# Performance work log

Hardware: AMD Instinct MI355X
Metric: run time of the kernel (lower is better)

## Reference

```python
import jax, jax.numpy as jnp
import numpy as np

B, L, D, H = 2, 2048, 1024, 16
DH = D // H  # 64

def setup_inputs() -> dict:
    key = jax.random.key(0)
    ks = jax.random.split(key, 5)
    s = 1.0 / np.sqrt(D)
    return {
        "x": jax.random.normal(ks[0], (B, L, D), jnp.float32),
        "Wk": jax.random.normal(ks[1], (D, D), jnp.float32) * s,
        "Wq": jax.random.normal(ks[2], (D, D), jnp.float32) * s,
        "Wv": jax.random.normal(ks[3], (D, D), jnp.float32) * s,
        "Wo": jax.random.normal(ks[4], (D, D), jnp.float32) * s,
    }

def reference(x, Wk, Wq, Wv, Wo):
    # Linear(D,D,bias=False): y = x @ W.T ; W stored [out,in] as in torch
    k = (x @ Wk.T).reshape(B, L, H, DH).transpose(0, 2, 1, 3)  # [B,H,L,dh]
    q = (x @ Wq.T).reshape(B, L, H, DH).transpose(0, 2, 1, 3)
    v = (x @ Wv.T).reshape(B, L, H, DH).transpose(0, 2, 1, 3)
    att = jnp.einsum("bhqd,bhkd->bhqk", q, k) / jnp.sqrt(jnp.float32(DH))
    causal = jnp.tril(jnp.ones((L, L), dtype=bool))
    att = jnp.where(causal, att, -jnp.inf)
    p = jax.nn.softmax(att, axis=-1)  # dropout omitted (eval mode)
    out = jnp.einsum("bhqk,bhkd->bhqd", p, v)  # [B,H,L,dh]
    out = out.transpose(0, 2, 1, 3).reshape(B, L, D)
    return out @ Wo.T
```

## Files before the change

### kernel.cpp

```cpp
#include <hip/hip_runtime.h>

typedef __bf16 bf16_t;
typedef __bf16 bf16x8 __attribute__((ext_vector_type(8)));
typedef __bf16 bf16x4 __attribute__((ext_vector_type(4)));
typedef float f32x4 __attribute__((ext_vector_type(4)));

#define MFMA_BF16(a, b, c) __builtin_amdgcn_mfma_f32_16x16x32_bf16((a), (b), (c), 0, 0, 0)
#define LOG2E 1.44269504088896f

__device__ __forceinline__ void gload16(const bf16_t* g, bf16_t* l) {
  __builtin_amdgcn_global_load_lds(
      (__attribute__((address_space(1))) void*)(g),
      (__attribute__((address_space(3))) void*)(l), 16, 0, 0);
}

__global__ void cast_all(const float* __restrict__ x, const float* __restrict__ wk,
                         const float* __restrict__ wq, const float* __restrict__ wv,
                         const float* __restrict__ wo, bf16_t* __restrict__ xbf,
                         bf16_t* __restrict__ wbf) {
  const size_t NX = 4194304, NW = 1048576;
  size_t i = (size_t)blockIdx.x * blockDim.x + threadIdx.x;
  const size_t total4 = (NX + 4 * NW) / 4;
  const size_t stride = (size_t)gridDim.x * blockDim.x;
  for (; i < total4; i += stride) {
    size_t f = i * 4;
    const float* src;
    bf16_t* dst;
    if (f < NX) {
      src = x + f;
      dst = xbf + f;
    } else {
      size_t g = f - NX;
      size_t wsel = g >> 20;
      size_t off = g & (NW - 1);
      dst = wbf + g;
      src = (wsel == 0) ? wq + off : (wsel == 1) ? wk + off : (wsel == 2) ? wv + off : wo + off;
    }
    float4 v = *(const float4*)src;
    bf16x4 o;
    o[0] = (bf16_t)v.x; o[1] = (bf16_t)v.y; o[2] = (bf16_t)v.z; o[3] = (bf16_t)v.w;
    *(bf16x4*)dst = o;
  }
}

template <int BM, int BN, typename TOUT>
__global__ __launch_bounds__(256) void gemm_nt(const bf16_t* __restrict__ A,
                                               const bf16_t* __restrict__ W,
                                               TOUT* __restrict__ C, int K, int ldc,
                                               int blocksPerSect, bf16_t* __restrict__ vtb) {
  constexpr int MF = BM / 32;
  constexpr int NF = BN / 32;
  __shared__ bf16_t As[BM * 64];
  __shared__ bf16_t Bs[BN * 64];
  const int t = threadIdx.x;
  const int l = t & 63, w = t >> 6;
  const int wm = w >> 1;
  const int wn = w & 1;
  const int lr = l & 15, lg = l >> 4;
  const int bm = blockIdx.x;
  const int by = blockIdx.y;
  const int sect = by / blocksPerSect;
  const int bn = by - sect * blocksPerSect;
  const bf16_t* Wp = W + ((size_t)sect << 20);
  const int n0 = sect * 1024 + bn * BN;

  const int srow0 = t >> 3;
  const int csw = (t & 7) ^ (srow0 & 7);
  const bf16_t* ag = A + (size_t)(bm * BM + srow0) * K + csw * 8;
  const bf16_t* bg = Wp + (size_t)(bn * BN + srow0) * K + csw * 8;

  f32x4 acc[MF][NF];
#pragma unroll
  for (int i = 0; i < MF; ++i)
#pragma unroll
    for (int j = 0; j < NF; ++j) acc[i][j] = (f32x4){0.f, 0.f, 0.f, 0.f};

  for (int k0 = 0; k0 < K; k0 += 64) {
    __syncthreads();
#pragma unroll
    for (int p = 0; p < BM / 32; ++p) gload16(ag + (size_t)(32 * p) * K, As + t * 8 + p * 2048);
#pragma unroll
    for (int p = 0; p < BN / 32; ++p) gload16(bg + (size_t)(32 * p) * K, Bs + t * 8 + p * 2048);
    ag += 64;
    bg += 64;
    __syncthreads();
#pragma unroll
    for (int kk = 0; kk < 2; ++kk) {
      bf16x8 af[MF], bfr[NF];
#pragma unroll
      for (int mf = 0; mf < MF; ++mf) {
        int row = wm * (MF * 16) + mf * 16 + lr;
        af[mf] = *(const bf16x8*)(As + row * 64 + (((kk * 4 + lg) ^ (row & 7)) * 8));
      }
#pragma unroll
      for (int nf = 0; nf < NF; ++nf) {
        int row = wn * (NF * 16) + nf * 16 + lr;
        bfr[nf] = *(const bf16x8*)(Bs + row * 64 + (((kk * 4 + lg) ^ (row & 7)) * 8));
      }
#pragma unroll
      for (int mf = 0; mf < MF; ++mf)
#pragma unroll
        for (int nf = 0; nf < NF; ++nf)
          acc[mf][nf] = MFMA_BF16(af[mf], bfr[nf], acc[mf][nf]);
    }
  }

  if (vtb != nullptr && sect == 2) {
#pragma unroll
    for (int mf = 0; mf < MF; ++mf)
#pragma unroll
      for (int nf = 0; nf < NF; ++nf) {
        int row0 = bm * BM + wm * (MF * 16) + mf * 16 + lg * 4;
        int colg = bn * BN + wn * (NF * 16) + nf * 16 + lr;
        int bb = row0 >> 11, ll = row0 & 2047;
        size_t vaddr = ((size_t)((bb * 16 + (colg >> 6)) * 64 + (colg & 63))) * 2048 + ll;
        bf16x4 pk;
#pragma unroll
        for (int j = 0; j < 4; ++j) pk[j] = (bf16_t)acc[mf][nf][j];
        *(bf16x4*)(vtb + vaddr) = pk;
      }
    return;
  }
#pragma unroll
  for (int mf = 0; mf < MF; ++mf)
#pragma unroll
    for (int nf = 0; nf < NF; ++nf)
#pragma unroll
      for (int j = 0; j < 4; ++j) {
        int row = bm * BM + wm * (MF * 16) + mf * 16 + lg * 4 + j;
        int col = n0 + wn * (NF * 16) + nf * 16 + lr;
        C[(size_t)row * ldc + col] = (TOUT)acc[mf][nf][j];
      }
}

__global__ __launch_bounds__(256, 4) void attn_fwd(const bf16_t* __restrict__ qk,
                                                   const bf16_t* __restrict__ vt,
                                                   bf16_t* __restrict__ out) {
  __shared__ bf16_t Ks[2][4096];
  __shared__ bf16_t Vts[2][4096];
  __shared__ bf16_t Pt[4][1024];
  const int t = threadIdx.x, l = t & 63, w = t >> 6;
  const int lr = l & 15, lg = l >> 4;
  const int n = blockIdx.x;
  const int bh = n & 31;
  const int b = bh >> 4, h = bh & 15;
  const int m = n >> 5;
  const int j8 = m & 7, kk = m >> 3;
  const int qt = (kk == 0) ? j8 : (kk == 1) ? 15 - j8 : (kk == 2) ? 16 + j8 : 31 - j8;
  const int qloc = w * 16 + lr;
  const int qrow = qt * 64 + qloc;

  const float SCINIT = -12.f * LOG2E;

  const int srow = t >> 3, sc8 = t & 7;
  const int cs = sc8 ^ (srow & 7);
  const bf16_t* kbase = qk + ((size_t)(b * 2048 + srow)) * 2048 + 1024 + h * 64 + cs * 8;
  const bf16_t* vbase = vt + ((size_t)(bh * 64 + srow)) * 2048 + cs * 8;
  char* Ks0 = (char*)&Ks[0][0];
  char* Vt0 = (char*)&Vts[0][0];
  const int stg = t * 16;

#define STAGE(ktile, sboff)                                                   \
  do {                                                                        \
    const bf16_t* ks_ = kbase + (size_t)(ktile) * (64 * 2048);                \
    const bf16_t* vs_ = vbase + (size_t)(ktile) * 64;                         \
    gload16(ks_, (bf16_t*)(Ks0 + (sboff) + stg));                             \
    gload16(ks_ + (size_t)32 * 2048, (bf16_t*)(Ks0 + (sboff) + 4096 + stg));  \
    gload16(vs_, (bf16_t*)(Vt0 + (sboff) + stg));                             \
    gload16(vs_ + (size_t)32 * 2048, (bf16_t*)(Vt0 + (sboff) + 4096 + stg));  \
  } while (0)

  const float qsc = 0.125f * LOG2E;
  const bf16_t* Qg = qk + (size_t)(b * 2048 + qrow) * 2048 + h * 64 + lg * 8;
  bf16x8 qf0 = *(const bf16x8*)(Qg);
  bf16x8 qf1 = *(const bf16x8*)(Qg + 32);
#pragma unroll
  for (int jj = 0; jj < 8; ++jj) {
    qf0[jj] = (bf16_t)((float)qf0[jj] * qsc);
    qf1[jj] = (bf16_t)((float)qf1[jj] * qsc);
  }

  f32x4 acc[4];
#pragma unroll
  for (int df = 0; df < 4; ++df) acc[df] = (f32x4){0.f, 0.f, 0.f, 0.f};
  float l_r = 0.f;

  const int r7 = lr & 7;
  const int o0 = lr * 128 + ((lg ^ r7) * 16);
  const int o1 = lr * 128 + (((lg ^ 4) ^ r7) * 16);

  char* PwB = (char*)&Pt[w][0];
  const int psw = r7 << 4;
  int pwo[4];
#pragma unroll
  for (int nf = 0; nf < 4; ++nf) pwo[nf] = lr * 128 + ((nf * 32 + lg * 8) ^ psw);
  const int pr0 = lr * 128 + ((lg * 16) ^ psw);
  const int pr1 = lr * 128 + ((64 + lg * 16) ^ psw);

  STAGE(0, 0);
  __syncthreads();

  int boff = 0;
  for (int kt = 0; kt <= qt; ++kt) {
    if (kt < qt) STAGE(kt + 1, boff ^ 8192);

    f32x4 sc[4];
#pragma unroll
    for (int nf = 0; nf < 4; ++nf)
      sc[nf] = (f32x4){SCINIT, SCINIT, SCINIT, SCINIT};
    __builtin_amdgcn_s_setprio(1);
#pragma unroll
    for (int nf = 0; nf < 4; ++nf) {
      bf16x8 kf0 = *(const bf16x8*)(Ks0 + boff + nf * 2048 + o0);
      bf16x8 kf1 = *(const bf16x8*)(Ks0 + boff + nf * 2048 + o1);
      sc[nf] = MFMA_BF16(kf0, qf0, sc[nf]);
      sc[nf] = MFMA_BF16(kf1, qf1, sc[nf]);
    }
    __builtin_amdgcn_s_setprio(0);

    float p[16], ps = 0.f;
    if (kt == qt) {
#pragma unroll
      for (int nf = 0; nf < 4; ++nf)
#pragma unroll
        for (int jj = 0; jj < 4; ++jj) {
          float sv = sc[nf][jj];
          if (nf * 16 + lg * 4 + jj > qloc) sv = -1e30f;
          float pv = __builtin_amdgcn_exp2f(sv);
          p[nf * 4 + jj] = pv;
          ps += pv;
        }
    } else {
#pragma unroll
      for (int nf = 0; nf < 4; ++nf)
#pragma unroll
        for (int jj = 0; jj < 4; ++jj) {
          float pv = __builtin_amdgcn_exp2f(sc[nf][jj]);
          p[nf * 4 + jj] = pv;
          ps += pv;
        }
    }
    l_r += ps;

#pragma unroll
    for (int nf = 0; nf < 4; ++nf) {
      bf16x4 pk;
#pragma unroll
      for (int jj = 0; jj < 4; ++jj) pk[jj] = (bf16_t)p[nf * 4 + jj];
      *(bf16x4*)(PwB + pwo[nf]) = pk;
    }

    bf16x8 pb0 = *(const bf16x8*)(PwB + pr0);
    bf16x8 pb1 = *(const bf16x8*)(PwB + pr1);
    __builtin_amdgcn_s_setprio(1);
#pragma unroll
    for (int df = 0; df < 4; ++df) {
      bf16x8 vf0 = *(const bf16x8*)(Vt0 + boff + df * 2048 + o0);
      bf16x8 vf1 = *(const bf16x8*)(Vt0 + boff + df * 2048 + o1);
      acc[df] = MFMA_BF16(vf0, pb0, acc[df]);
      acc[df] = MFMA_BF16(vf1, pb1, acc[df]);
    }
    __builtin_amdgcn_s_setprio(0);
    __syncthreads();
    boff ^= 8192;
  }
#undef STAGE

  l_r += __shfl_xor(l_r, 16);
  l_r += __shfl_xor(l_r, 32);
  float inv = 1.f / l_r;
#pragma unroll
  for (int df = 0; df < 4; ++df) {
    bf16x4 o;
#pragma unroll
    for (int jj = 0; jj < 4; ++jj) o[jj] = (bf16_t)(acc[df][jj] * inv);
    *(bf16x4*)(out + (size_t)(b * 2048 + qrow) * 1024 + h * 64 + df * 16 + lg * 4) = o;
  }
}

extern "C" void kernel_launch(void* const* d_in, const int* in_sizes, int n_in,
                              void* d_out, int out_size, void* d_ws, size_t ws_size,
                              hipStream_t stream) {
  const float* x = (const float*)d_in[0];
  const float* wk = (const float*)d_in[1];
  const float* wq = (const float*)d_in[2];
  const float* wv = (const float*)d_in[3];
  const float* wo = (const float*)d_in[4];

  bf16_t* xbf = (bf16_t*)d_ws;
  bf16_t* wbf = xbf + 4194304;
  bf16_t* qkbf = wbf + 4194304;
  bf16_t* vtbuf = qkbf + 8388608;
  bf16_t* attnbf = xbf;
  float* out = (float*)d_out;

  cast_all<<<dim3(2048), dim3(256), 0, stream>>>(x, wk, wq, wv, wo, xbf, wbf);
  gemm_nt<128, 64, bf16_t><<<dim3(32, 48), dim3(256), 0, stream>>>(xbf, wbf, qkbf, 1024, 2048, 16,
                                                                   vtbuf);
  attn_fwd<<<dim3(1024), dim3(256), 0, stream>>>(qkbf, vtbuf, attnbf);
  gemm_nt<64, 64, float><<<dim3(64, 16), dim3(256), 0, stream>>>(attnbf, wbf + 3 * 1048576, out,
                                                                 1024, 1024, 16, (bf16_t*)nullptr);
}
```

Measured before the change: 102.4 us.

## Double-buffer GEMM LDS tiles with K-step 32 and prefetch next stage

Changes the projection GEMM main loop from a single-buffered 64-wide K tile to two 32-wide K tile buffers. The next stage's global-to-LDS loads are issued before computing on the current buffer, leaving one barrier per iteration. This aims to overlap memory latency with MFMA work. In exchange it halves the MFMA work per iteration, doubles the iteration count and changes the LDS swizzle.

```diff
diff --git a/kernel.cpp b/kernel.cpp
--- a/kernel.cpp
+++ b/kernel.cpp
@@ -50,8 +50,10 @@
                                                int blocksPerSect, bf16_t* __restrict__ vtb) {
   constexpr int MF = BM / 32;
   constexpr int NF = BN / 32;
-  __shared__ bf16_t As[BM * 64];
-  __shared__ bf16_t Bs[BN * 64];
+  constexpr int ABYTES = BM * 64;
+  constexpr int BBYTES = BN * 64;
+  __shared__ bf16_t As[2][BM * 32];
+  __shared__ bf16_t Bs[2][BN * 32];
   const int t = threadIdx.x;
   const int l = t & 63, w = t >> 6;
   const int wm = w >> 1;
@@ -64,10 +66,25 @@
   const bf16_t* Wp = W + ((size_t)sect << 20);
   const int n0 = sect * 1024 + bn * BN;
 
-  const int srow0 = t >> 3;
-  const int csw = (t & 7) ^ (srow0 & 7);
+  const int srow0 = t >> 2;
+  const int csw = (t & 3) ^ ((t >> 3) & 3);
   const bf16_t* ag = A + (size_t)(bm * BM + srow0) * K + csw * 8;
   const bf16_t* bg = Wp + (size_t)(bn * BN + srow0) * K + csw * 8;
+  char* As0 = (char*)&As[0][0];
+  char* Bs0 = (char*)&Bs[0][0];
+  const int stg = t * 16;
+
+#define GSTAGE(k0, sb)                                                                   \
+  do {                                                                                   \
+    _Pragma("unroll") for (int p = 0; p < BM / 64; ++p)                                  \
+        gload16(ag + (size_t)(64 * p) * K + (k0), (bf16_t*)(As0 + (sb)*ABYTES + p * 4096 + stg)); \
+    _Pragma("unroll") for (int p = 0; p < BN / 64; ++p)                                  \
+        gload16(bg + (size_t)(64 * p) * K + (k0), (bf16_t*)(Bs0 + (sb)*BBYTES + p * 4096 + stg)); \
+  } while (0)
+
+  const int off = lr * 64 + ((lg ^ ((lr >> 1) & 3)) * 16);
+  const int abase = wm * (MF * 1024) + off;
+  const int bbase = wn * (NF * 1024) + off;
 
   f32x4 acc[MF][NF];
 #pragma unroll
@@ -75,35 +92,28 @@
 #pragma unroll
     for (int j = 0; j < NF; ++j) acc[i][j] = (f32x4){0.f, 0.f, 0.f, 0.f};
 
-  for (int k0 = 0; k0 < K; k0 += 64) {
+  GSTAGE(0, 0);
+  __syncthreads();
+
+  int cb = 0;
+  for (int k0 = 0; k0 < K; k0 += 32) {
+    if (k0 + 32 < K) GSTAGE(k0 + 32, cb ^ 1);
+    bf16x8 af[MF], bfr[NF];
+#pragma unroll
+    for (int mf = 0; mf < MF; ++mf)
+      af[mf] = *(const bf16x8*)(As0 + cb * ABYTES + abase + mf * 1024);
+#pragma unroll
+    for (int nf = 0; nf < NF; ++nf)
+      bfr[nf] = *(const bf16x8*)(Bs0 + cb * BBYTES + bbase + nf * 1024);
+#pragma unroll
+    for (int mf = 0; mf < MF; ++mf)
+#pragma unroll
+      for (int nf = 0; nf < NF; ++nf)
+        acc[mf][nf] = MFMA_BF16(af[mf], bfr[nf], acc[mf][nf]);
     __syncthreads();
-#pragma unroll
-    for (int p = 0; p < BM / 32; ++p) gload16(ag + (size_t)(32 * p) * K, As + t * 8 + p * 2048);
-#pragma unroll
-    for (int p = 0; p < BN / 32; ++p) gload16(bg + (size_t)(32 * p) * K, Bs + t * 8 + p * 2048);
-    ag += 64;
-    bg += 64;
-    __syncthreads();
-#pragma unroll
-    for (int kk = 0; kk < 2; ++kk) {
-      bf16x8 af[MF], bfr[NF];
-#pragma unroll
-      for (int mf = 0; mf < MF; ++mf) {
-        int row = wm * (MF * 16) + mf * 16 + lr;
-        af[mf] = *(const bf16x8*)(As + row * 64 + (((kk * 4 + lg) ^ (row & 7)) * 8));
-      }
-#pragma unroll
-      for (int nf = 0; nf < NF; ++nf) {
-        int row = wn * (NF * 16) + nf * 16 + lr;
-        bfr[nf] = *(const bf16x8*)(Bs + row * 64 + (((kk * 4 + lg) ^ (row & 7)) * 8));
-      }
-#pragma unroll
-      for (int mf = 0; mf < MF; ++mf)
-#pragma unroll
-        for (int nf = 0; nf < NF; ++nf)
-          acc[mf][nf] = MFMA_BF16(af[mf], bfr[nf], acc[mf][nf]);
-    }
-  }
+    cb ^= 1;
+  }
+#undef GSTAGE
 
   if (vtb != nullptr && sect == 2) {
 #pragma unroll
```

Result: slower. 111.6 us (+9.0%).
